# Kernel tuning notes

Hardware: AMD Instinct MI355X
Metric: run time of the kernel (lower is better)

## Reference

```python
import jax, jax.numpy as jnp
import numpy as np

EXP_CLAMP = 1.0e6
DENOM_EPS = 1e-10
LRELU_ALPHA = 0.01


def setup_inputs() -> dict:
    key = jax.random.key(0)
    k1, k2, k3, k4, k5, k6 = jax.random.split(key, 6)
    B, N, E, F = 4, 16384, 262144, 64
    h = jax.random.normal(k1, (B, N, F), dtype=jnp.float32)
    edge = jax.random.randint(k2, (B, E, 2), 0, N, dtype=jnp.int32)
    edge_num = jax.random.randint(k3, (B,), 1, E, dtype=jnp.int32)
    edge_weight = jax.random.uniform(k4, (B, E), dtype=jnp.float32)
    W = jax.random.normal(k5, (F, F), dtype=jnp.float32) * 0.15  # xavier-ish scale
    a = jax.random.normal(k6, (1, 2 * F), dtype=jnp.float32) * 0.12
    return {"h": h, "edge": edge, "edge_num": edge_num,
            "edge_weight": edge_weight, "W": W, "a": a}


def _seg_sum(src, idx, num_segments):
    # src: [E, ...], idx: [E] -> [num_segments, ...]
    return jax.ops.segment_sum(src, idx, num_segments=num_segments)


def reference(h, edge, edge_num, edge_weight, W, a):
    B, N, Fin = h.shape
    E = edge.shape[1]
    # linear transform: Wh = h @ W^T  -> [B, N, Fout]
    Wh = jnp.einsum('bnf,of->bno', h, W)
    ctr = edge[:, :, 0]  # [B, E]
    nbr = edge[:, :, 1]  # [B, E]
    Wh_c = jnp.take_along_axis(Wh, ctr[:, :, None], axis=1)  # [B, E, Fout]
    Wh_n = jnp.take_along_axis(Wh, nbr[:, :, None], axis=1)  # [B, E, Fout]
    a_input = jnp.concatenate([Wh_c, Wh_n], axis=-1) * edge_weight[:, :, None]
    # attention logits: leakyrelu(a_input @ a^T), squeeze to [B, E]
    att1 = jax.nn.leaky_relu(jnp.einsum('bek,k->be', a_input, a[0]), LRELU_ALPHA)
    # per-batch valid-edge mask (edges beyond edge_num zeroed, as in torch loop)
    mask = (jnp.arange(E, dtype=jnp.int32)[None, :] < edge_num[:, None])
    x_exp = jnp.clip(jnp.exp(att1), 0.0, EXP_CLAMP) * mask.astype(att1.dtype)
    # segment softmax denominator over center nodes
    denom = DENOM_EPS + jax.vmap(_seg_sum, in_axes=(0, 0, None))(x_exp, ctr, N)  # [B, N]
    att = x_exp / jnp.take_along_axis(denom, ctr, axis=1)  # [B, E]
    # weighted neighbor aggregation via scatter-add on center index
    att_Wh = Wh_n * att[:, :, None]  # masked edges already have att == 0
    h_prime = jax.vmap(_seg_sum, in_axes=(0, 0, None))(att_Wh, ctr, N)  # [B, N, Fout]
    return jax.nn.relu(h_prime)
```

## Files before the change

kernel.cpp:

```cpp
#include <hip/hip_runtime.h>

#define BB 4
#define NN 16384
#define EE 262144
#define FF 64
#define ROWS (BB * NN)
#define CAP 64
#define CHUNKS 64
#define CHUNK_E (EE / CHUNKS)
#define TILE_R 256

typedef __bf16 bf16x8 __attribute__((ext_vector_type(8)));
typedef float  f32x4  __attribute__((ext_vector_type(4)));

__device__ __forceinline__ unsigned short f32_to_bf16(float f) {
    unsigned int u = __float_as_uint(f);
    u += 0x7FFFu + ((u >> 16) & 1u);
    return (unsigned short)(u >> 16);
}

__global__ __launch_bounds__(256) void mfma_kernel(
    const float* __restrict__ h, const float* __restrict__ W,
    const float* __restrict__ a,
    unsigned short* __restrict__ Wh,
    float* __restrict__ sc, float* __restrict__ sn)
{
    __shared__ float wc[FF], wn[FF];
    const int t = threadIdx.x;
    const int lane = t & 63;
    const int m = lane & 15;
    const int q = lane >> 4;

    if (t < 128) {
        const int f = t & 63;
        const float* av = a + (t >> 6) * FF;
        float s = 0.0f;
        #pragma unroll 8
        for (int o = 0; o < FF; ++o)
            s = fmaf(av[o], W[o * FF + f], s);
        (t < 64 ? wc : wn)[f] = s;
    }

    bf16x8 bfrag[4][2];
    #pragma unroll
    for (int nt = 0; nt < 4; ++nt) {
        const float* wr = W + (nt * 16 + m) * FF;
        #pragma unroll
        for (int kh = 0; kh < 2; ++kh) {
            const float4 v0 = *(const float4*)(wr + kh * 32 + q * 8);
            const float4 v1 = *(const float4*)(wr + kh * 32 + q * 8 + 4);
            bf16x8 b;
            b[0] = (__bf16)v0.x; b[1] = (__bf16)v0.y;
            b[2] = (__bf16)v0.z; b[3] = (__bf16)v0.w;
            b[4] = (__bf16)v1.x; b[5] = (__bf16)v1.y;
            b[6] = (__bf16)v1.z; b[7] = (__bf16)v1.w;
            bfrag[nt][kh] = b;
        }
    }

    __syncthreads();

    const int waveId = (blockIdx.x * 256 + t) >> 6;
    const int R0 = waveId * 16;
    const float* hr = h + (size_t)(R0 + m) * FF;
    bf16x8 af[2];
    float s1 = 0.0f, s2 = 0.0f;
    #pragma unroll
    for (int kh = 0; kh < 2; ++kh) {
        const float4 v0 = *(const float4*)(hr + kh * 32 + q * 8);
        const float4 v1 = *(const float4*)(hr + kh * 32 + q * 8 + 4);
        bf16x8 aa;
        aa[0] = (__bf16)v0.x; aa[1] = (__bf16)v0.y;
        aa[2] = (__bf16)v0.z; aa[3] = (__bf16)v0.w;
        aa[4] = (__bf16)v1.x; aa[5] = (__bf16)v1.y;
        aa[6] = (__bf16)v1.z; aa[7] = (__bf16)v1.w;
        af[kh] = aa;
        const int fb = kh * 32 + q * 8;
        const float4 c0 = *(const float4*)&wc[fb];
        const float4 c1 = *(const float4*)&wc[fb + 4];
        const float4 n0 = *(const float4*)&wn[fb];
        const float4 n1 = *(const float4*)&wn[fb + 4];
        s1 = fmaf(v0.x, c0.x, fmaf(v0.y, c0.y, fmaf(v0.z, c0.z, fmaf(v0.w, c0.w, s1))));
        s1 = fmaf(v1.x, c1.x, fmaf(v1.y, c1.y, fmaf(v1.z, c1.z, fmaf(v1.w, c1.w, s1))));
        s2 = fmaf(v0.x, n0.x, fmaf(v0.y, n0.y, fmaf(v0.z, n0.z, fmaf(v0.w, n0.w, s2))));
        s2 = fmaf(v1.x, n1.x, fmaf(v1.y, n1.y, fmaf(v1.z, n1.z, fmaf(v1.w, n1.w, s2))));
    }
    s1 += __shfl_xor(s1, 16); s2 += __shfl_xor(s2, 16);
    s1 += __shfl_xor(s1, 32); s2 += __shfl_xor(s2, 32);
    if (lane < 16) { sc[R0 + m] = s1; sn[R0 + m] = s2; }

    #pragma unroll
    for (int nt = 0; nt < 4; ++nt) {
        f32x4 acc = {0.f, 0.f, 0.f, 0.f};
        acc = __builtin_amdgcn_mfma_f32_16x16x32_bf16(af[0], bfrag[nt][0], acc, 0, 0, 0);
        acc = __builtin_amdgcn_mfma_f32_16x16x32_bf16(af[1], bfrag[nt][1], acc, 0, 0, 0);
        #pragma unroll
        for (int i = 0; i < 4; ++i)
            Wh[(size_t)(R0 + q * 4 + i) * FF + nt * 16 + m] = f32_to_bf16(acc[i]);
    }
}

__global__ __launch_bounds__(256) void hist_kernel(
    const int* __restrict__ edge, const int* __restrict__ edge_num,
    unsigned int* __restrict__ histG)
{
    __shared__ unsigned int hist[NN];
    const int g = blockIdx.x;
    const int b = g >> 6, c = g & (CHUNKS - 1);
    const int t = threadIdx.x;
    const int en = edge_num[b];
    const int e0 = c * CHUNK_E;
    unsigned int* outp = histG + (size_t)g * NN;

    if (e0 >= en) {
        for (int r = t; r < NN; r += 256) outp[r] = 0u;
        return;
    }
    for (int r = t; r < NN; r += 256) hist[r] = 0u;
    __syncthreads();

    const int2* ep = (const int2*)edge + (size_t)b * EE + e0;
    const int nAct = min(en - e0, CHUNK_E);
    for (int j = t; j < nAct; j += 256)
        atomicAdd(&hist[ep[j].x], 1u);
    __syncthreads();

    for (int r = t; r < NN; r += 256) outp[r] = hist[r];
}

__global__ __launch_bounds__(256) void scan_kernel(
    unsigned int* __restrict__ histG, int* __restrict__ cnt)
{
    __shared__ unsigned int tile[CHUNKS][TILE_R];
    const int g = blockIdx.x;
    const int b = g >> 6, tl = g & 63;
    const int r0 = tl * TILE_R;
    const int t = threadIdx.x;

    #pragma unroll 8
    for (int c = 0; c < CHUNKS; ++c)
        tile[c][t] = histG[(size_t)(b * CHUNKS + c) * NN + r0 + t];
    __syncthreads();

    unsigned int acc = 0;
    #pragma unroll 8
    for (int c = 0; c < CHUNKS; ++c) {
        const unsigned int v = tile[c][t];
        tile[c][t] = acc;
        acc += v;
    }
    cnt[b * NN + r0 + t] = (int)acc;

    #pragma unroll 8
    for (int c = 0; c < CHUNKS; ++c)
        histG[(size_t)(b * CHUNKS + c) * NN + r0 + t] = tile[c][t];
}

__global__ __launch_bounds__(256) void scatter_kernel(
    const int* __restrict__ edge, const int* __restrict__ edge_num,
    const unsigned int* __restrict__ baseG,
    unsigned int* __restrict__ payload)
{
    __shared__ unsigned int hist[NN];
    const int g = blockIdx.x;
    const int b = g >> 6, c = g & (CHUNKS - 1);
    const int t = threadIdx.x;
    const int en = edge_num[b];
    const int e0 = c * CHUNK_E;
    if (e0 >= en) return;

    for (int r = t; r < NN; r += 256) hist[r] = 0u;
    __syncthreads();

    const unsigned int* base = baseG + (size_t)(b * CHUNKS + c) * NN;
    const int2* ep = (const int2*)edge + (size_t)b * EE + e0;
    const int nAct = min(en - e0, CHUNK_E);
    unsigned int* payB = payload + (size_t)b * NN * CAP;

    for (int j = t; j < nAct; j += 256) {
        const int2 e2 = ep[j];
        const unsigned int rank = atomicAdd(&hist[e2.x], 1u);
        const unsigned int slot = base[e2.x] + rank;
        const unsigned int eid  = (unsigned int)(e0 + j);
        if (slot < CAP)
            payB[(size_t)e2.x * CAP + slot] = (eid << 14) | (unsigned int)e2.y;
    }
}

__global__ __launch_bounds__(256) void gather_kernel(
    const int* __restrict__ cnt, const unsigned int* __restrict__ payload,
    const uint2* __restrict__ Wh2,
    const float* __restrict__ sc, const float* __restrict__ sn,
    const float* __restrict__ ew,
    float* __restrict__ out)
{
    const int bi = blockIdx.x;
    const int xcd = bi & 7;
    const int batch = xcd >> 1;
    const int within = ((bi >> 3) << 1) | (xcd & 1);
    const int rg = batch * 4096 + within;

    const int lane = threadIdx.x & 63;
    const int wave = threadIdx.x >> 6;
    const int row = rg * 4 + wave;
    const int grp = lane >> 4;
    const int gl  = lane & 15;
    int deg = cnt[row];
    if (deg > CAP) deg = CAP;
    const unsigned int* pl = payload + (size_t)row * CAP;
    const uint2* WhB = Wh2 + (size_t)batch * NN * 16;
    const float* snB = sn + batch * NN;
    const float* ewB = ew + (size_t)batch * EE;
    const float scr = sc[row];

    unsigned int p = 0u;
    if (lane < deg) {
        const unsigned int raw = pl[lane];
        const float s0 = ewB[raw >> 14] * (scr + snB[raw & 0x3FFFu]);
        const float s1 = s0 > 0.0f ? s0 : 0.01f * s0;
        const float xe = fminf(__expf(s1), 1000000.0f);
        p = ((__float_as_uint(xe) + 0x2000u) & 0xFFFFC000u) | (raw & 0x3FFFu);
    }

    float a0 = 0.f, a1 = 0.f, a2 = 0.f, a3 = 0.f, dsum = 0.f;
    for (int jj = 0; jj < deg; jj += 16) {
        const unsigned int pv0 = __shfl(p, jj + grp);
        const unsigned int pv1 = __shfl(p, jj + grp + 4);
        const unsigned int pv2 = __shfl(p, jj + grp + 8);
        const unsigned int pv3 = __shfl(p, jj + grp + 12);
        const uint2 w0 = WhB[(size_t)(pv0 & 0x3FFFu) * 16 + gl];
        const uint2 w1 = WhB[(size_t)(pv1 & 0x3FFFu) * 16 + gl];
        const uint2 w2 = WhB[(size_t)(pv2 & 0x3FFFu) * 16 + gl];
        const uint2 w3 = WhB[(size_t)(pv3 & 0x3FFFu) * 16 + gl];
        const float xe0 = __uint_as_float(pv0 & 0xFFFFC000u);
        const float xe1 = __uint_as_float(pv1 & 0xFFFFC000u);
        const float xe2 = __uint_as_float(pv2 & 0xFFFFC000u);
        const float xe3 = __uint_as_float(pv3 & 0xFFFFC000u);
        a0 = fmaf(xe0, __uint_as_float(w0.x << 16),         a0);
        a1 = fmaf(xe0, __uint_as_float(w0.x & 0xFFFF0000u), a1);
        a2 = fmaf(xe0, __uint_as_float(w0.y << 16),         a2);
        a3 = fmaf(xe0, __uint_as_float(w0.y & 0xFFFF0000u), a3);
        a0 = fmaf(xe1, __uint_as_float(w1.x << 16),         a0);
        a1 = fmaf(xe1, __uint_as_float(w1.x & 0xFFFF0000u), a1);
        a2 = fmaf(xe1, __uint_as_float(w1.y << 16),         a2);
        a3 = fmaf(xe1, __uint_as_float(w1.y & 0xFFFF0000u), a3);
        a0 = fmaf(xe2, __uint_as_float(w2.x << 16),         a0);
        a1 = fmaf(xe2, __uint_as_float(w2.x & 0xFFFF0000u), a1);
        a2 = fmaf(xe2, __uint_as_float(w2.y << 16),         a2);
        a3 = fmaf(xe2, __uint_as_float(w2.y & 0xFFFF0000u), a3);
        a0 = fmaf(xe3, __uint_as_float(w3.x << 16),         a0);
        a1 = fmaf(xe3, __uint_as_float(w3.x & 0xFFFF0000u), a1);
        a2 = fmaf(xe3, __uint_as_float(w3.y << 16),         a2);
        a3 = fmaf(xe3, __uint_as_float(w3.y & 0xFFFF0000u), a3);
        dsum += (xe0 + xe1) + (xe2 + xe3);
    }
    a0 += __shfl_xor(a0, 16); a1 += __shfl_xor(a1, 16);
    a2 += __shfl_xor(a2, 16); a3 += __shfl_xor(a3, 16);
    dsum += __shfl_xor(dsum, 16);
    a0 += __shfl_xor(a0, 32); a1 += __shfl_xor(a1, 32);
    a2 += __shfl_xor(a2, 32); a3 += __shfl_xor(a3, 32);
    dsum += __shfl_xor(dsum, 32);

    if (grp == 0) {
        const float inv = 1.0f / (1e-10f + dsum);
        float4 o;
        o.x = fmaxf(a0 * inv, 0.0f);
        o.y = fmaxf(a1 * inv, 0.0f);
        o.z = fmaxf(a2 * inv, 0.0f);
        o.w = fmaxf(a3 * inv, 0.0f);
        ((float4*)out)[(size_t)row * 16 + gl] = o;
    }
}

extern "C" void kernel_launch(void* const* d_in, const int* in_sizes, int n_in,
                              void* d_out, int out_size, void* d_ws, size_t ws_size,
                              hipStream_t stream)
{
    const float* h        = (const float*)d_in[0];
    const int*   edge     = (const int*)  d_in[1];
    const int*   edge_num = (const int*)  d_in[2];
    const float* ew       = (const float*)d_in[3];
    const float* W        = (const float*)d_in[4];
    const float* a        = (const float*)d_in[5];
    float* out = (float*)d_out;

    unsigned short* Wh = (unsigned short*)d_ws;
    float* sc        = (float*)(Wh + (size_t)BB * NN * FF);
    float* sn        = sc + ROWS;
    int*   cnt       = (int*)(sn + ROWS);
    unsigned int* payload = (unsigned int*)(cnt + ROWS);
    unsigned int* histG   = payload + (size_t)ROWS * CAP;

    mfma_kernel<<<1024, 256, 0, stream>>>(h, W, a, Wh, sc, sn);

    hist_kernel<<<BB * CHUNKS, 256, 0, stream>>>(edge, edge_num, histG);

    scan_kernel<<<BB * (NN / TILE_R), 256, 0, stream>>>(histG, cnt);

    scatter_kernel<<<BB * CHUNKS, 256, 0, stream>>>(edge, edge_num,
                                                    histG, payload);

    gather_kernel<<<ROWS / 4, 256, 0, stream>>>(cnt, payload,
                                                (const uint2*)Wh,
                                                sc, sn, ew, out);
}
```

Before: 149.0 us.

## Shrink histogram to 16-bit, skip inactive chunks, preload scatter bases into LDS

Per-chunk histograms and exclusive bases are now stored as 16-bit values, halving the histogram traffic written and read by the hist, scan and scatter kernels. The scan kernel loops only over chunks that contain valid edges, using edge_num. The scatter kernel loads its base offsets into shared memory once and uses one LDS atomic per edge, replacing the separate rank counter and the global base read. The gather kernel loads the payload and computes the attention value unconditionally and masks the result afterwards, removing a divergent branch around the loads. Bases are clamped at 65535, which is only safe while per-node degree stays small. The gather now reads payload slots that were never written (harmless, since those lanes are masked).

After: 141.2 us. 5.2% less time.

```diff
diff --git a/kernel.cpp b/kernel.cpp
--- a/kernel.cpp
+++ b/kernel.cpp
@@ -102,64 +102,7 @@
 
 __global__ __launch_bounds__(256) void hist_kernel(
     const int* __restrict__ edge, const int* __restrict__ edge_num,
-    unsigned int* __restrict__ histG)
-{
-    __shared__ unsigned int hist[NN];
-    const int g = blockIdx.x;
-    const int b = g >> 6, c = g & (CHUNKS - 1);
-    const int t = threadIdx.x;
-    const int en = edge_num[b];
-    const int e0 = c * CHUNK_E;
-    unsigned int* outp = histG + (size_t)g * NN;
-
-    if (e0 >= en) {
-        for (int r = t; r < NN; r += 256) outp[r] = 0u;
-        return;
-    }
-    for (int r = t; r < NN; r += 256) hist[r] = 0u;
-    __syncthreads();
-
-    const int2* ep = (const int2*)edge + (size_t)b * EE + e0;
-    const int nAct = min(en - e0, CHUNK_E);
-    for (int j = t; j < nAct; j += 256)
-        atomicAdd(&hist[ep[j].x], 1u);
-    __syncthreads();
-
-    for (int r = t; r < NN; r += 256) outp[r] = hist[r];
-}
-
-__global__ __launch_bounds__(256) void scan_kernel(
-    unsigned int* __restrict__ histG, int* __restrict__ cnt)
-{
-    __shared__ unsigned int tile[CHUNKS][TILE_R];
-    const int g = blockIdx.x;
-    const int b = g >> 6, tl = g & 63;
-    const int r0 = tl * TILE_R;
-    const int t = threadIdx.x;
-
-    #pragma unroll 8
-    for (int c = 0; c < CHUNKS; ++c)
-        tile[c][t] = histG[(size_t)(b * CHUNKS + c) * NN + r0 + t];
-    __syncthreads();
-
-    unsigned int acc = 0;
-    #pragma unroll 8
-    for (int c = 0; c < CHUNKS; ++c) {
-        const unsigned int v = tile[c][t];
-        tile[c][t] = acc;
-        acc += v;
-    }
-    cnt[b * NN + r0 + t] = (int)acc;
-
-    #pragma unroll 8
-    for (int c = 0; c < CHUNKS; ++c)
-        histG[(size_t)(b * CHUNKS + c) * NN + r0 + t] = tile[c][t];
-}
-
-__global__ __launch_bounds__(256) void scatter_kernel(
-    const int* __restrict__ edge, const int* __restrict__ edge_num,
-    const unsigned int* __restrict__ baseG,
-    unsigned int* __restrict__ payload)
+    unsigned short* __restrict__ histG)
 {
     __shared__ unsigned int hist[NN];
     const int g = blockIdx.x;
@@ -172,15 +115,77 @@
     for (int r = t; r < NN; r += 256) hist[r] = 0u;
     __syncthreads();
 
-    const unsigned int* base = baseG + (size_t)(b * CHUNKS + c) * NN;
+    const int2* ep = (const int2*)edge + (size_t)b * EE + e0;
+    const int nAct = min(en - e0, CHUNK_E);
+    for (int j = t; j < nAct; j += 256)
+        atomicAdd(&hist[ep[j].x], 1u);
+    __syncthreads();
+
+    ushort2* out2 = (ushort2*)(histG + (size_t)g * NN);
+    for (int r2 = t; r2 < NN / 2; r2 += 256) {
+        ushort2 v;
+        v.x = (unsigned short)hist[2 * r2];
+        v.y = (unsigned short)hist[2 * r2 + 1];
+        out2[r2] = v;
+    }
+}
+
+__global__ __launch_bounds__(256) void scan_kernel(
+    const int* __restrict__ edge_num,
+    unsigned short* __restrict__ histG, int* __restrict__ cnt)
+{
+    __shared__ unsigned short tile[CHUNKS][TILE_R];
+    const int g = blockIdx.x;
+    const int b = g >> 6, tl = g & 63;
+    const int r0 = tl * TILE_R;
+    const int t = threadIdx.x;
+    const int en = edge_num[b];
+    const int nact = min((en + CHUNK_E - 1) / CHUNK_E, CHUNKS);
+
+    for (int c = 0; c < nact; ++c)
+        tile[c][t] = histG[(size_t)(b * CHUNKS + c) * NN + r0 + t];
+    __syncthreads();
+
+    unsigned int acc = 0;
+    for (int c = 0; c < nact; ++c) {
+        const unsigned int v = tile[c][t];
+        tile[c][t] = (unsigned short)(acc > 65535u ? 65535u : acc);
+        acc += v;
+    }
+    cnt[b * NN + r0 + t] = (int)acc;
+
+    for (int c = 0; c < nact; ++c)
+        histG[(size_t)(b * CHUNKS + c) * NN + r0 + t] = tile[c][t];
+}
+
+__global__ __launch_bounds__(256) void scatter_kernel(
+    const int* __restrict__ edge, const int* __restrict__ edge_num,
+    const unsigned short* __restrict__ baseG,
+    unsigned int* __restrict__ payload)
+{
+    __shared__ unsigned int slotA[NN];
+    const int g = blockIdx.x;
+    const int b = g >> 6, c = g & (CHUNKS - 1);
+    const int t = threadIdx.x;
+    const int en = edge_num[b];
+    const int e0 = c * CHUNK_E;
+    if (e0 >= en) return;
+
+    const ushort2* b2 = (const ushort2*)(baseG + (size_t)(b * CHUNKS + c) * NN);
+    for (int r2 = t; r2 < NN / 2; r2 += 256) {
+        const ushort2 v = b2[r2];
+        slotA[2 * r2]     = v.x;
+        slotA[2 * r2 + 1] = v.y;
+    }
+    __syncthreads();
+
     const int2* ep = (const int2*)edge + (size_t)b * EE + e0;
     const int nAct = min(en - e0, CHUNK_E);
     unsigned int* payB = payload + (size_t)b * NN * CAP;
 
     for (int j = t; j < nAct; j += 256) {
         const int2 e2 = ep[j];
-        const unsigned int rank = atomicAdd(&hist[e2.x], 1u);
-        const unsigned int slot = base[e2.x] + rank;
+        const unsigned int slot = atomicAdd(&slotA[e2.x], 1u);
         const unsigned int eid  = (unsigned int)(e0 + j);
         if (slot < CAP)
             payB[(size_t)e2.x * CAP + slot] = (eid << 14) | (unsigned int)e2.y;
@@ -205,22 +210,22 @@
     const int row = rg * 4 + wave;
     const int grp = lane >> 4;
     const int gl  = lane & 15;
-    int deg = cnt[row];
-    if (deg > CAP) deg = CAP;
     const unsigned int* pl = payload + (size_t)row * CAP;
     const uint2* WhB = Wh2 + (size_t)batch * NN * 16;
     const float* snB = sn + batch * NN;
     const float* ewB = ew + (size_t)batch * EE;
+
+    int deg = cnt[row];
+    const unsigned int praw = pl[lane];
     const float scr = sc[row];
-
-    unsigned int p = 0u;
-    if (lane < deg) {
-        const unsigned int raw = pl[lane];
-        const float s0 = ewB[raw >> 14] * (scr + snB[raw & 0x3FFFu]);
-        const float s1 = s0 > 0.0f ? s0 : 0.01f * s0;
-        const float xe = fminf(__expf(s1), 1000000.0f);
-        p = ((__float_as_uint(xe) + 0x2000u) & 0xFFFFC000u) | (raw & 0x3FFFu);
-    }
+    if (deg > CAP) deg = CAP;
+
+    const float s0 = ewB[praw >> 14] * (scr + snB[praw & 0x3FFFu]);
+    const float s1 = s0 > 0.0f ? s0 : 0.01f * s0;
+    const float xe = fminf(__expf(s1), 1000000.0f);
+    const unsigned int p = (lane < deg)
+        ? (((__float_as_uint(xe) + 0x2000u) & 0xFFFFC000u) | (praw & 0x3FFFu))
+        : 0u;
 
     float a0 = 0.f, a1 = 0.f, a2 = 0.f, a3 = 0.f, dsum = 0.f;
     for (int jj = 0; jj < deg; jj += 16) {
@@ -289,13 +294,13 @@
     float* sn        = sc + ROWS;
     int*   cnt       = (int*)(sn + ROWS);
     unsigned int* payload = (unsigned int*)(cnt + ROWS);
-    unsigned int* histG   = payload + (size_t)ROWS * CAP;
+    unsigned short* histG = (unsigned short*)(payload + (size_t)ROWS * CAP);
 
     mfma_kernel<<<1024, 256, 0, stream>>>(h, W, a, Wh, sc, sn);
 
     hist_kernel<<<BB * CHUNKS, 256, 0, stream>>>(edge, edge_num, histG);
 
-    scan_kernel<<<BB * (NN / TILE_R), 256, 0, stream>>>(histG, cnt);
+    scan_kernel<<<BB * (NN / TILE_R), 256, 0, stream>>>(edge_num, histG, cnt);
 
     scatter_kernel<<<BB * CHUNKS, 256, 0, stream>>>(edge, edge_num,
                                                     histG, payload);
```
